# Kernel optimization log

Measured on AMD Instinct MI355X. Metric: run time of the kernel, lower is better.

The kernel has to match this reference:

```python
import jax, jax.numpy as jnp
import numpy as np

N = 50000   # nodes
E = 800000  # random edges (self-loops appended inside reference, as PyG GATConv does)
H = 4       # attention heads
LEAKY_SLOPE = 0.2
BN_EPS = 1e-5


def setup_inputs() -> dict:
    key = jax.random.key(0)
    ks = jax.random.split(key, 24)
    inp = {
        "x": jax.random.normal(ks[0], (N, 128), jnp.float32),
        "edge_index": jax.random.randint(ks[1], (2, E), 0, N, dtype=jnp.int64),
    }
    # layer dims: (in, out_per_head); concat -> out width = H*out
    dims = [(128, 64), (256, 64), (256, 32)]
    i = 2
    for l, (fin, c) in enumerate(dims, start=1):
        sc = 1.0 / np.sqrt(fin)
        inp[f"W{l}"] = jax.random.normal(ks[i], (fin, H * c), jnp.float32) * sc; i += 1
        inp[f"a_src{l}"] = jax.random.normal(ks[i], (H, c), jnp.float32) * 0.1; i += 1
        inp[f"a_dst{l}"] = jax.random.normal(ks[i], (H, c), jnp.float32) * 0.1; i += 1
        inp[f"b{l}"] = jnp.zeros((H * c,), jnp.float32)
    # batch norm params for the two non-final layers (width = 64*4 = 256)
    for l in (1, 2):
        inp[f"gamma{l}"] = jnp.ones((256,), jnp.float32)
        inp[f"beta{l}"] = jnp.zeros((256,), jnp.float32)
    return inp


def _gat_layer(x, src, dst, W, a_src, a_dst, b, heads):
    n = x.shape[0]
    h = (x @ W).reshape(n, heads, -1)                      # [N,H,C]
    al_s = jnp.sum(h * a_src, axis=-1)                     # [N,H]
    al_d = jnp.sum(h * a_dst, axis=-1)                     # [N,H]
    e = jax.nn.leaky_relu(al_s[src] + al_d[dst], LEAKY_SLOPE)  # [Etot,H]
    # numerically-stable edge softmax over incoming edges per destination
    m = jax.ops.segment_max(e, dst, num_segments=n)
    e = jnp.exp(e - m[dst])
    s = jax.ops.segment_sum(e, dst, num_segments=n)
    alpha = e / (s[dst] + 1e-16)                           # [Etot,H]
    msg = alpha[:, :, None] * h[src]                       # [Etot,H,C]
    out = jax.ops.segment_sum(msg, dst, num_segments=n)    # [N,H,C]
    out = out.reshape(n, -1) + b
    return jax.nn.relu(out)  # GAT_NET applies relu after conv


def _batch_norm(x, gamma, beta):
    mean = jnp.mean(x, axis=0)
    var = jnp.var(x, axis=0)  # biased, matches torch BN training normalization
    return (x - mean) * jax.lax.rsqrt(var + BN_EPS) * gamma + beta


def reference(x, edge_index, W1, a_src1, a_dst1, b1, gamma1, beta1,
              W2, a_src2, a_dst2, b2, gamma2, beta2,
              W3, a_src3, a_dst3, b3):
    n = x.shape[0]
    loop = jnp.arange(n, dtype=edge_index.dtype)
    src = jnp.concatenate([edge_index[0], loop])  # add self-loops (PyG default)
    dst = jnp.concatenate([edge_index[1], loop])

    h = _gat_layer(x, src, dst, W1, a_src1, a_dst1, b1, H)
    # outer F.relu is a no-op after GAT_NET's internal relu, kept implicitly
    h = _batch_norm(h, gamma1, beta1)

    h = _gat_layer(h, src, dst, W2, a_src2, a_dst2, b2, H)
    h = _batch_norm(h, gamma2, beta2)

    return _gat_layer(h, src, dst, W3, a_src3, a_dst3, b3, H)
```

## Files before the change

kernel.cpp:

```cpp
#include <hip/hip_runtime.h>
#include <hip/hip_bf16.h>

constexpr int NN   = 50000;
constexpr int EE   = 800000;
constexpr int ETOT = EE + NN;
constexpr int NP   = 50048;
constexpr int NBLK = (NN + 255) / 256;
constexpr float SLOPE  = 0.2f;
constexpr float EPS_BN = 1e-5f;

typedef __attribute__((ext_vector_type(8))) short bf16x8;
typedef __attribute__((ext_vector_type(4))) float f32x4;

__device__ inline float bf2f(unsigned short u) {
    union { unsigned int i; float f; } c; c.i = ((unsigned int)u) << 16; return c.f;
}

__device__ inline void gload16(const __hip_bfloat16* g, __hip_bfloat16* l) {
    __builtin_amdgcn_global_load_lds(
        (const __attribute__((address_space(1))) unsigned int*)g,
        (__attribute__((address_space(3))) unsigned int*)l, 16, 0, 0);
}


__global__ __launch_bounds__(256) void count_kernel(const int* __restrict__ ei,
                                                    int* __restrict__ cnt) {
    int j = blockIdx.x * 256 + threadIdx.x;
    if (j >= ETOT) return;
    int dst = (j < EE) ? ei[EE + j] : (j - EE);
    atomicAdd(&cnt[dst], 1);
}

__global__ __launch_bounds__(256) void scanA_kernel(const int* __restrict__ cnt,
                                                    int* __restrict__ off,
                                                    int* __restrict__ bsum) {
    int b = blockIdx.x, t = threadIdx.x;
    int i = b * 256 + t;
    int v = (i < NN) ? cnt[i] : 0;
    int lane = t & 63, w = t >> 6;
    int x = v;
    #pragma unroll
    for (int o = 1; o < 64; o <<= 1) { int y = __shfl_up(x, o); if (lane >= o) x += y; }
    __shared__ int ws[4];
    if (lane == 63) ws[w] = x;
    __syncthreads();
    int wo = 0;
    for (int k = 0; k < w; ++k) wo += ws[k];
    int incl = x + wo;
    if (i < NN) off[i] = incl - v;
    if (t == 255) bsum[b] = incl;
}

__global__ __launch_bounds__(256) void scanB_kernel(const int* __restrict__ bsum,
                                                    int* __restrict__ bexc,
                                                    int* __restrict__ off) {
    int t = threadIdx.x;
    int v = (t < NBLK) ? bsum[t] : 0;
    int lane = t & 63, w = t >> 6;
    int x = v;
    #pragma unroll
    for (int o = 1; o < 64; o <<= 1) { int y = __shfl_up(x, o); if (lane >= o) x += y; }
    __shared__ int ws[4];
    if (lane == 63) ws[w] = x;
    __syncthreads();
    int wo = 0;
    for (int k = 0; k < w; ++k) wo += ws[k];
    int incl = x + wo;
    if (t < NBLK) bexc[t] = incl - v;
    if (t == 255) off[NN] = incl;
}

__global__ __launch_bounds__(256) void scanC_kernel(const int* __restrict__ bexc,
                                                    int* __restrict__ off,
                                                    int* __restrict__ cur) {
    int i = blockIdx.x * 256 + threadIdx.x;
    if (i >= NN) return;
    int v = off[i] + bexc[blockIdx.x];
    off[i] = v;
    cur[i] = v;
}

__global__ __launch_bounds__(256) void fill_kernel(const int* __restrict__ ei,
                                                   int* __restrict__ cursor,
                                                   int* __restrict__ ssrc) {
    int j = blockIdx.x * 256 + threadIdx.x;
    if (j >= ETOT) return;
    int src, dst;
    if (j < EE) { src = ei[j]; dst = ei[EE + j]; }
    else        { src = dst = j - EE; }
    int pos = atomicAdd(&cursor[dst], 1);
    ssrc[pos] = src;
}

__global__ __launch_bounds__(256) void castx_kernel(const float* __restrict__ X,
                                                    __hip_bfloat16* __restrict__ Xbf) {
    long e0 = ((long)blockIdx.x * 256 + threadIdx.x) * 8;
    if (e0 >= (long)NP * 128) return;
    int row = (int)(e0 / 128);
    __hip_bfloat16 o[8];
    if (row < NN) {
        float4 v0 = *reinterpret_cast<const float4*>(X + e0);
        float4 v1 = *reinterpret_cast<const float4*>(X + e0 + 4);
        o[0] = __float2bfloat16(v0.x); o[1] = __float2bfloat16(v0.y);
        o[2] = __float2bfloat16(v0.z); o[3] = __float2bfloat16(v0.w);
        o[4] = __float2bfloat16(v1.x); o[5] = __float2bfloat16(v1.y);
        o[6] = __float2bfloat16(v1.z); o[7] = __float2bfloat16(v1.w);
    } else {
        for (int j = 0; j < 8; ++j) o[j] = __float2bfloat16(0.f);
    }
    *reinterpret_cast<bf16x8*>(Xbf + e0) = *reinterpret_cast<bf16x8*>(o);
}

__global__ __launch_bounds__(256) void castw1_kernel(const float* __restrict__ W,
                                                     __hip_bfloat16* __restrict__ WT) {
    int i = blockIdx.x * 256 + threadIdx.x;
    if (i >= 32768) return;
    int c = i / 128, k = i % 128;
    WT[i] = __float2bfloat16(W[(size_t)k * 256 + c]);
}

template <int FIN, int WOUT>
__global__ __launch_bounds__(FIN) void foldw_kernel(const float* __restrict__ W,
                                                    const float* __restrict__ scale,
                                                    const float* __restrict__ shift,
                                                    __hip_bfloat16* __restrict__ WTp,
                                                    float* __restrict__ bb) {
    int c = blockIdx.x, k = threadIdx.x;
    float w = W[(size_t)k * WOUT + c];
    WTp[(size_t)c * FIN + k] = __float2bfloat16(scale[k] * w);
    float p = shift[k] * w;
    #pragma unroll
    for (int o = 1; o < 64; o <<= 1) p += __shfl_xor(p, o);
    __shared__ float ps[FIN / 64];
    if ((k & 63) == 0) ps[k >> 6] = p;
    __syncthreads();
    if (k == 0) {
        float s = 0.f;
        #pragma unroll
        for (int q = 0; q < FIN / 64; ++q) s += ps[q];
        bb[c] = s;
    }
}

template <int FIN, int WOUT, bool FOLD>
__global__ __launch_bounds__(256) void mgemm_kernel(const __hip_bfloat16* __restrict__ A,
                                                    const __hip_bfloat16* __restrict__ BT,
                                                    const float* __restrict__ bb,
                                                    __hip_bfloat16* __restrict__ Hbf) {
    __shared__ __hip_bfloat16 As[128 * 32];
    __shared__ __hip_bfloat16 Bs[128 * 32];
    int t = threadIdx.x;
    int lane = t & 63, w = t >> 6;
    int row0 = blockIdx.x * 128;
    int col0 = blockIdx.y * 128;
    int wr = w >> 1, wc = w & 1;

    f32x4 acc[4][4];
    #pragma unroll
    for (int m = 0; m < 4; ++m)
        #pragma unroll
        for (int n = 0; n < 4; ++n) acc[m][n] = (f32x4){0.f, 0.f, 0.f, 0.f};

    int srow = w * 32 + (lane >> 2);
    int sbc  = (lane & 3) * 8;
    const __hip_bfloat16* gA0 = A  + (size_t)(row0 + srow)      * FIN + sbc;
    const __hip_bfloat16* gA1 = A  + (size_t)(row0 + srow + 16) * FIN + sbc;
    const __hip_bfloat16* gB0 = BT + (size_t)(col0 + srow)      * FIN + sbc;
    const __hip_bfloat16* gB1 = BT + (size_t)(col0 + srow + 16) * FIN + sbc;
    __hip_bfloat16* lA0 = As + w * 1024;
    __hip_bfloat16* lA1 = As + w * 1024 + 512;
    __hip_bfloat16* lB0 = Bs + w * 1024;
    __hip_bfloat16* lB1 = Bs + w * 1024 + 512;

    int rA = (wr * 64 + (lane & 15)) * 32 + (lane >> 4) * 8;
    int rB = (wc * 64 + (lane & 15)) * 32 + (lane >> 4) * 8;

    for (int k0 = 0; k0 < FIN; k0 += 32) {
        gload16(gA0 + k0, lA0);
        gload16(gA1 + k0, lA1);
        gload16(gB0 + k0, lB0);
        gload16(gB1 + k0, lB1);
        __syncthreads();
        bf16x8 af[4], bfr[4];
        #pragma unroll
        for (int m = 0; m < 4; ++m) af[m]  = *reinterpret_cast<const bf16x8*>(As + rA + m * 16 * 32);
        #pragma unroll
        for (int n = 0; n < 4; ++n) bfr[n] = *reinterpret_cast<const bf16x8*>(Bs + rB + n * 16 * 32);
        #pragma unroll
        for (int m = 0; m < 4; ++m)
            #pragma unroll
            for (int n = 0; n < 4; ++n)
                acc[m][n] = __builtin_amdgcn_mfma_f32_16x16x32_bf16(af[m], bfr[n], acc[m][n], 0, 0, 0);
        __syncthreads();
    }

    #pragma unroll
    for (int n = 0; n < 4; ++n) {
        int c = col0 + wc * 64 + n * 16 + (lane & 15);
        float badd = FOLD ? bb[c] : 0.f;
        #pragma unroll
        for (int m = 0; m < 4; ++m) {
            int r = row0 + wr * 64 + m * 16 + (lane >> 4) * 4;
            #pragma unroll
            for (int j = 0; j < 4; ++j)
                Hbf[(size_t)(r + j) * WOUT + c] = __float2bfloat16(acc[m][n][j] + badd);
        }
    }
}

template <int HC>
__global__ __launch_bounds__(256) void alsd_kernel(const __hip_bfloat16* __restrict__ Hm,
                                                   const float* __restrict__ a_src,
                                                   const float* __restrict__ a_dst,
                                                   float* __restrict__ als,
                                                   float* __restrict__ ald) {
    constexpr int VW = HC / 64;
    int wid  = threadIdx.x >> 6;
    int lane = threadIdx.x & 63;
    int node = blockIdx.x * 4 + wid;

    float ssum = 0.f, dsum = 0.f;
    if constexpr (VW == 4) {
        ushort4 h4 = *reinterpret_cast<const ushort4*>(Hm + (size_t)node * HC + lane * 4);
        float4 as = *reinterpret_cast<const float4*>(a_src + lane * 4);
        float4 ad = *reinterpret_cast<const float4*>(a_dst + lane * 4);
        float hx = bf2f(h4.x), hy = bf2f(h4.y), hz = bf2f(h4.z), hw = bf2f(h4.w);
        ssum = hx*as.x + hy*as.y + hz*as.z + hw*as.w;
        dsum = hx*ad.x + hy*ad.y + hz*ad.z + hw*ad.w;
    } else {
        ushort2 h2 = *reinterpret_cast<const ushort2*>(Hm + (size_t)node * HC + lane * 2);
        float2 as = *reinterpret_cast<const float2*>(a_src + lane * 2);
        float2 ad = *reinterpret_cast<const float2*>(a_dst + lane * 2);
        float hx = bf2f(h2.x), hy = bf2f(h2.y);
        ssum = hx*as.x + hy*as.y;
        dsum = hx*ad.x + hy*ad.y;
    }
    #pragma unroll
    for (int o = 1; o < 16; o <<= 1) {
        ssum += __shfl_xor(ssum, o);
        dsum += __shfl_xor(dsum, o);
    }
    if ((lane & 15) == 0) {
        int hd = lane >> 4;
        als[node * 4 + hd] = ssum;
        ald[node * 4 + hd] = dsum;
    }
}

template <int HC, bool OUTBF>
__global__ __launch_bounds__(256) void attn_kernel(const __hip_bfloat16* __restrict__ Hm,
                                                   const int* __restrict__ off,
                                                   const int* __restrict__ ssrc,
                                                   const float* __restrict__ als,
                                                   const float* __restrict__ ald,
                                                   const float* __restrict__ bias,
                                                   void* __restrict__ Outv) {
    constexpr int CPL = HC / 16;
    int wid  = threadIdx.x >> 6;
    int lane = threadIdx.x & 63;
    int d    = blockIdx.x * 4 + wid;
    int g    = lane >> 4;
    int q    = lane & 15;
    int head = q >> 2;

    int e0 = off[d], e1 = off[d + 1];
    float aldh = ald[(size_t)d * 4 + head];

    float acc0[CPL], acc1[CPL];
    #pragma unroll
    for (int c = 0; c < CPL; ++c) { acc0[c] = 0.f; acc1[c] = 0.f; }
    float den0 = 0.f, den1 = 0.f;

    int j = e0 + g;
    for (; j + 4 < e1; j += 8) {
        int s0 = ssrc[j];
        int s1 = ssrc[j + 4];
        float ea = als[(size_t)s0 * 4 + head] + aldh;
        ea = (ea > 0.f) ? ea : SLOPE * ea;
        float eb = als[(size_t)s1 * 4 + head] + aldh;
        eb = (eb > 0.f) ? eb : SLOPE * eb;
        float w0 = __expf(ea), w1 = __expf(eb);
        den0 += w0; den1 += w1;
        const __hip_bfloat16* hp0 = Hm + (size_t)s0 * HC + q * CPL;
        const __hip_bfloat16* hp1 = Hm + (size_t)s1 * HC + q * CPL;
        if constexpr (CPL == 16) {
            bf16x8 a0 = *reinterpret_cast<const bf16x8*>(hp0);
            bf16x8 a1 = *reinterpret_cast<const bf16x8*>(hp0 + 8);
            bf16x8 b0 = *reinterpret_cast<const bf16x8*>(hp1);
            bf16x8 b1 = *reinterpret_cast<const bf16x8*>(hp1 + 8);
            #pragma unroll
            for (int c = 0; c < 8; ++c) {
                acc0[c]     += w0 * bf2f((unsigned short)a0[c]);
                acc0[8 + c] += w0 * bf2f((unsigned short)a1[c]);
                acc1[c]     += w1 * bf2f((unsigned short)b0[c]);
                acc1[8 + c] += w1 * bf2f((unsigned short)b1[c]);
            }
        } else {
            bf16x8 a0 = *reinterpret_cast<const bf16x8*>(hp0);
            bf16x8 b0 = *reinterpret_cast<const bf16x8*>(hp1);
            #pragma unroll
            for (int c = 0; c < 8; ++c) {
                acc0[c] += w0 * bf2f((unsigned short)a0[c]);
                acc1[c] += w1 * bf2f((unsigned short)b0[c]);
            }
        }
    }
    if (j < e1) {
        int s0 = ssrc[j];
        float ea = als[(size_t)s0 * 4 + head] + aldh;
        ea = (ea > 0.f) ? ea : SLOPE * ea;
        float w0 = __expf(ea);
        den0 += w0;
        const __hip_bfloat16* hp0 = Hm + (size_t)s0 * HC + q * CPL;
        if constexpr (CPL == 16) {
            bf16x8 a0 = *reinterpret_cast<const bf16x8*>(hp0);
            bf16x8 a1 = *reinterpret_cast<const bf16x8*>(hp0 + 8);
            #pragma unroll
            for (int c = 0; c < 8; ++c) {
                acc0[c]     += w0 * bf2f((unsigned short)a0[c]);
                acc0[8 + c] += w0 * bf2f((unsigned short)a1[c]);
            }
        } else {
            bf16x8 a0 = *reinterpret_cast<const bf16x8*>(hp0);
            #pragma unroll
            for (int c = 0; c < 8; ++c) acc0[c] += w0 * bf2f((unsigned short)a0[c]);
        }
    }

    float den = den0 + den1;
    float acc[CPL];
    #pragma unroll
    for (int c = 0; c < CPL; ++c) acc[c] = acc0[c] + acc1[c];

    #pragma unroll
    for (int c = 0; c < CPL; ++c) {
        acc[c] += __shfl_xor(acc[c], 16);
        acc[c] += __shfl_xor(acc[c], 32);
    }
    den += __shfl_xor(den, 16);
    den += __shfl_xor(den, 32);
    float inv = 1.f / (den + 1e-16f);

    if (g == 0) {
        float o[CPL];
        #pragma unroll
        for (int c4 = 0; c4 < CPL / 4; ++c4) {
            float4 b4 = *reinterpret_cast<const float4*>(bias + q * CPL + c4 * 4);
            o[c4 * 4 + 0] = fmaxf(acc[c4 * 4 + 0] * inv + b4.x, 0.f);
            o[c4 * 4 + 1] = fmaxf(acc[c4 * 4 + 1] * inv + b4.y, 0.f);
            o[c4 * 4 + 2] = fmaxf(acc[c4 * 4 + 2] * inv + b4.z, 0.f);
            o[c4 * 4 + 3] = fmaxf(acc[c4 * 4 + 3] * inv + b4.w, 0.f);
        }
        if constexpr (OUTBF) {
            __hip_bfloat16 ob[CPL];
            #pragma unroll
            for (int c = 0; c < CPL; ++c) ob[c] = __float2bfloat16(o[c]);
            __hip_bfloat16* op = (__hip_bfloat16*)Outv + (size_t)d * HC + q * CPL;
            #pragma unroll
            for (int c8 = 0; c8 < CPL / 8; ++c8)
                *reinterpret_cast<bf16x8*>(op + c8 * 8) = *reinterpret_cast<bf16x8*>(ob + c8 * 8);
        } else {
            float* op = (float*)Outv + (size_t)d * HC + q * CPL;
            #pragma unroll
            for (int c4 = 0; c4 < CPL / 4; ++c4)
                *reinterpret_cast<float4*>(op + c4 * 4) =
                    make_float4(o[c4*4+0], o[c4*4+1], o[c4*4+2], o[c4*4+3]);
        }
    }
}

__global__ __launch_bounds__(256) void bnstats_kernel(const __hip_bfloat16* __restrict__ X,
                                                      float* __restrict__ sums) {
    int c  = threadIdx.x;
    int r0 = blockIdx.x * 200;
    float s = 0.f, q = 0.f;
    for (int r = r0; r < r0 + 200; ++r) {
        float v = bf2f(*(const unsigned short*)(X + (size_t)r * 256 + c));
        s += v; q += v * v;
    }
    atomicAdd(&sums[c], s);
    atomicAdd(&sums[256 + c], q);
}

__global__ __launch_bounds__(256) void bnfinal_kernel(const float* __restrict__ sums,
                                                      const float* __restrict__ gamma,
                                                      const float* __restrict__ beta,
                                                      float* __restrict__ scale,
                                                      float* __restrict__ shift) {
    int c = threadIdx.x;
    float mean = sums[c] / (float)NN;
    float var  = sums[256 + c] / (float)NN - mean * mean;
    float inv  = rsqrtf(var + EPS_BN);
    float sc   = gamma[c] * inv;
    scale[c] = sc;
    shift[c] = beta[c] - mean * sc;
}


extern "C" void kernel_launch(void* const* d_in, const int* in_sizes, int n_in,
                              void* d_out, int out_size, void* d_ws, size_t ws_size,
                              hipStream_t stream) {
    const float* x      = (const float*)d_in[0];
    const int*   ei     = (const int*)d_in[1];
    const float* W1     = (const float*)d_in[2];
    const float* a_s1   = (const float*)d_in[3];
    const float* a_d1   = (const float*)d_in[4];
    const float* b1     = (const float*)d_in[5];
    const float* W2     = (const float*)d_in[6];
    const float* a_s2   = (const float*)d_in[7];
    const float* a_d2   = (const float*)d_in[8];
    const float* b2     = (const float*)d_in[9];
    const float* W3     = (const float*)d_in[10];
    const float* a_s3   = (const float*)d_in[11];
    const float* a_d3   = (const float*)d_in[12];
    const float* b3     = (const float*)d_in[13];
    const float* gamma1 = (const float*)d_in[14];
    const float* beta1  = (const float*)d_in[15];
    const float* gamma2 = (const float*)d_in[16];
    const float* beta2  = (const float*)d_in[17];

    char* ws = (char*)d_ws;
    size_t o = 0;
    auto alloc = [&](size_t bytes) -> void* {
        void* p = ws + o;
        o = (o + bytes + 255) & ~size_t(255);
        return p;
    };
    __hip_bfloat16*  Abf  = (__hip_bfloat16*)alloc((size_t)NP * 256 * 2);
    __hip_bfloat16*  Hbf  = (__hip_bfloat16*)alloc((size_t)NP * 256 * 2);
    __hip_bfloat16*  Xbf  = (__hip_bfloat16*)alloc((size_t)NP * 128 * 2);
    __hip_bfloat16*  WT1  = (__hip_bfloat16*)alloc((size_t)256 * 128 * 2);
    __hip_bfloat16*  WT2  = (__hip_bfloat16*)alloc((size_t)256 * 256 * 2);
    __hip_bfloat16*  WT3  = (__hip_bfloat16*)alloc((size_t)128 * 256 * 2);
    float* bb2   = (float*)alloc(256 * 4);
    float* bb3   = (float*)alloc(128 * 4);
    float* als   = (float*)alloc((size_t)NN * 4 * 4);
    float* ald   = (float*)alloc((size_t)NN * 4 * 4);
    float* sums  = (float*)alloc(512 * 4);
    float* scale = (float*)alloc(256 * 4);
    float* shift = (float*)alloc(256 * 4);
    int*   off   = (int*)alloc((size_t)(NN + 1) * 4);
    int*   cur   = (int*)alloc((size_t)NN * 4);
    int*   cnt   = (int*)alloc((size_t)NN * 4);
    int*   bsum  = (int*)alloc((size_t)NBLK * 4);
    int*   bexc  = (int*)alloc((size_t)NBLK * 4);
    int*   ssrc  = (int*)alloc((size_t)ETOT * 4);
    (void)ws_size; (void)in_sizes; (void)n_in; (void)out_size;

    const int EB = (ETOT + 255) / 256;

    hipMemsetAsync(cnt, 0, (size_t)NN * 4, stream);
    count_kernel<<<EB, 256, 0, stream>>>(ei, cnt);
    scanA_kernel<<<NBLK, 256, 0, stream>>>(cnt, off, bsum);
    scanB_kernel<<<1, 256, 0, stream>>>(bsum, bexc, off);
    scanC_kernel<<<NBLK, 256, 0, stream>>>(bexc, off, cur);
    fill_kernel<<<EB, 256, 0, stream>>>(ei, cur, ssrc);

    castw1_kernel<<<128, 256, 0, stream>>>(W1, WT1);
    castx_kernel<<<(int)(((long)NP * 128 / 8 + 255) / 256), 256, 0, stream>>>(x, Xbf);
    mgemm_kernel<128, 256, false><<<dim3(NP / 128, 2), 256, 0, stream>>>(Xbf, WT1, nullptr, Hbf);
    alsd_kernel<256><<<NN / 4, 256, 0, stream>>>(Hbf, a_s1, a_d1, als, ald);
    attn_kernel<256, true><<<NN / 4, 256, 0, stream>>>(Hbf, off, ssrc, als, ald, b1, Abf);

    hipMemsetAsync(sums, 0, 512 * 4, stream);
    bnstats_kernel<<<250, 256, 0, stream>>>(Abf, sums);
    bnfinal_kernel<<<1, 256, 0, stream>>>(sums, gamma1, beta1, scale, shift);
    foldw_kernel<256, 256><<<256, 256, 0, stream>>>(W2, scale, shift, WT2, bb2);

    mgemm_kernel<256, 256, true><<<dim3(NP / 128, 2), 256, 0, stream>>>(Abf, WT2, bb2, Hbf);
    alsd_kernel<256><<<NN / 4, 256, 0, stream>>>(Hbf, a_s2, a_d2, als, ald);
    attn_kernel<256, true><<<NN / 4, 256, 0, stream>>>(Hbf, off, ssrc, als, ald, b2, Abf);

    hipMemsetAsync(sums, 0, 512 * 4, stream);
    bnstats_kernel<<<250, 256, 0, stream>>>(Abf, sums);
    bnfinal_kernel<<<1, 256, 0, stream>>>(sums, gamma2, beta2, scale, shift);
    foldw_kernel<256, 128><<<128, 256, 0, stream>>>(W3, scale, shift, WT3, bb3);

    mgemm_kernel<256, 128, true><<<dim3(NP / 128, 1), 256, 0, stream>>>(Abf, WT3, bb3, Hbf);
    alsd_kernel<128><<<NN / 4, 256, 0, stream>>>(Hbf, a_s3, a_d3, als, ald);
    attn_kernel<128, false><<<NN / 4, 256, 0, stream>>>(Hbf, off, ssrc, als, ald, b3, d_out);
}
```

Baseline: 402.5 us.

## Fuse attention-logit dot products into GEMM epilogue; one node per 16-lane group

Result: faster. 385.0 us (-4.3%).

```diff
diff --git a/kernel.cpp b/kernel.cpp
--- a/kernel.cpp
+++ b/kernel.cpp
@@ -146,7 +146,11 @@
 __global__ __launch_bounds__(256) void mgemm_kernel(const __hip_bfloat16* __restrict__ A,
                                                     const __hip_bfloat16* __restrict__ BT,
                                                     const float* __restrict__ bb,
-                                                    __hip_bfloat16* __restrict__ Hbf) {
+                                                    const float* __restrict__ a_src,
+                                                    const float* __restrict__ a_dst,
+                                                    __hip_bfloat16* __restrict__ Hbf,
+                                                    float* __restrict__ als,
+                                                    float* __restrict__ ald) {
     __shared__ __hip_bfloat16 As[128 * 32];
     __shared__ __hip_bfloat16 Bs[128 * 32];
     int t = threadIdx.x;
@@ -194,56 +198,86 @@
         __syncthreads();
     }
 
+    int cih = lane & 15;
+
+    if constexpr (FOLD) {
+        #pragma unroll
+        for (int n = 0; n < 4; ++n) {
+            float badd = bb[col0 + wc * 64 + n * 16 + cih];
+            #pragma unroll
+            for (int m = 0; m < 4; ++m)
+                #pragma unroll
+                for (int j = 0; j < 4; ++j) acc[m][n][j] += badd;
+        }
+    }
+
+    float asv[4], adv[4];
+    int headw = 0;
+    if constexpr (WOUT == 256) {
+        headw = (col0 >> 6) + wc;
+        #pragma unroll
+        for (int n = 0; n < 4; ++n) {
+            asv[n] = a_src[headw * 64 + n * 16 + cih];
+            adv[n] = a_dst[headw * 64 + n * 16 + cih];
+        }
+    } else {
+        #pragma unroll
+        for (int n = 0; n < 4; ++n) {
+            int hh = wc * 2 + (n >> 1);
+            asv[n] = a_src[hh * 32 + (n & 1) * 16 + cih];
+            adv[n] = a_dst[hh * 32 + (n & 1) * 16 + cih];
+        }
+    }
+
+    #pragma unroll
+    for (int m = 0; m < 4; ++m) {
+        #pragma unroll
+        for (int j = 0; j < 4; ++j) {
+            int r = row0 + wr * 64 + m * 16 + (lane >> 4) * 4 + j;
+            if constexpr (WOUT == 256) {
+                float vs = acc[m][0][j] * asv[0] + acc[m][1][j] * asv[1]
+                         + acc[m][2][j] * asv[2] + acc[m][3][j] * asv[3];
+                float vd = acc[m][0][j] * adv[0] + acc[m][1][j] * adv[1]
+                         + acc[m][2][j] * adv[2] + acc[m][3][j] * adv[3];
+                #pragma unroll
+                for (int o = 1; o < 16; o <<= 1) {
+                    vs += __shfl_xor(vs, o);
+                    vd += __shfl_xor(vd, o);
+                }
+                if (cih == 0) {
+                    als[(size_t)r * 4 + headw] = vs;
+                    ald[(size_t)r * 4 + headw] = vd;
+                }
+            } else {
+                float vs0 = acc[m][0][j] * asv[0] + acc[m][1][j] * asv[1];
+                float vs1 = acc[m][2][j] * asv[2] + acc[m][3][j] * asv[3];
+                float vd0 = acc[m][0][j] * adv[0] + acc[m][1][j] * adv[1];
+                float vd1 = acc[m][2][j] * adv[2] + acc[m][3][j] * adv[3];
+                #pragma unroll
+                for (int o = 1; o < 16; o <<= 1) {
+                    vs0 += __shfl_xor(vs0, o); vs1 += __shfl_xor(vs1, o);
+                    vd0 += __shfl_xor(vd0, o); vd1 += __shfl_xor(vd1, o);
+                }
+                if (cih == 0) {
+                    als[(size_t)r * 4 + wc * 2]     = vs0;
+                    als[(size_t)r * 4 + wc * 2 + 1] = vs1;
+                    ald[(size_t)r * 4 + wc * 2]     = vd0;
+                    ald[(size_t)r * 4 + wc * 2 + 1] = vd1;
+                }
+            }
+        }
+    }
+
     #pragma unroll
     for (int n = 0; n < 4; ++n) {
-        int c = col0 + wc * 64 + n * 16 + (lane & 15);
-        float badd = FOLD ? bb[c] : 0.f;
+        int c = col0 + wc * 64 + n * 16 + cih;
         #pragma unroll
         for (int m = 0; m < 4; ++m) {
             int r = row0 + wr * 64 + m * 16 + (lane >> 4) * 4;
             #pragma unroll
             for (int j = 0; j < 4; ++j)
-                Hbf[(size_t)(r + j) * WOUT + c] = __float2bfloat16(acc[m][n][j] + badd);
-        }
-    }
-}
-
-template <int HC>
-__global__ __launch_bounds__(256) void alsd_kernel(const __hip_bfloat16* __restrict__ Hm,
-                                                   const float* __restrict__ a_src,
-                                                   const float* __restrict__ a_dst,
-                                                   float* __restrict__ als,
-                                                   float* __restrict__ ald) {
-    constexpr int VW = HC / 64;
-    int wid  = threadIdx.x >> 6;
-    int lane = threadIdx.x & 63;
-    int node = blockIdx.x * 4 + wid;
-
-    float ssum = 0.f, dsum = 0.f;
-    if constexpr (VW == 4) {
-        ushort4 h4 = *reinterpret_cast<const ushort4*>(Hm + (size_t)node * HC + lane * 4);
-        float4 as = *reinterpret_cast<const float4*>(a_src + lane * 4);
-        float4 ad = *reinterpret_cast<const float4*>(a_dst + lane * 4);
-        float hx = bf2f(h4.x), hy = bf2f(h4.y), hz = bf2f(h4.z), hw = bf2f(h4.w);
-        ssum = hx*as.x + hy*as.y + hz*as.z + hw*as.w;
-        dsum = hx*ad.x + hy*ad.y + hz*ad.z + hw*ad.w;
-    } else {
-        ushort2 h2 = *reinterpret_cast<const ushort2*>(Hm + (size_t)node * HC + lane * 2);
-        float2 as = *reinterpret_cast<const float2*>(a_src + lane * 2);
-        float2 ad = *reinterpret_cast<const float2*>(a_dst + lane * 2);
-        float hx = bf2f(h2.x), hy = bf2f(h2.y);
-        ssum = hx*as.x + hy*as.y;
-        dsum = hx*ad.x + hy*ad.y;
-    }
-    #pragma unroll
-    for (int o = 1; o < 16; o <<= 1) {
-        ssum += __shfl_xor(ssum, o);
-        dsum += __shfl_xor(dsum, o);
-    }
-    if ((lane & 15) == 0) {
-        int hd = lane >> 4;
-        als[node * 4 + hd] = ssum;
-        ald[node * 4 + hd] = dsum;
+                Hbf[(size_t)(r + j) * WOUT + c] = __float2bfloat16(acc[m][n][j]);
+        }
     }
 }
 
@@ -258,114 +292,110 @@
     constexpr int CPL = HC / 16;
     int wid  = threadIdx.x >> 6;
     int lane = threadIdx.x & 63;
-    int d    = blockIdx.x * 4 + wid;
     int g    = lane >> 4;
     int q    = lane & 15;
+    int d    = blockIdx.x * 16 + wid * 4 + g;
     int head = q >> 2;
 
     int e0 = off[d], e1 = off[d + 1];
     float aldh = ald[(size_t)d * 4 + head];
 
-    float acc0[CPL], acc1[CPL];
-    #pragma unroll
-    for (int c = 0; c < CPL; ++c) { acc0[c] = 0.f; acc1[c] = 0.f; }
-    float den0 = 0.f, den1 = 0.f;
-
-    int j = e0 + g;
-    for (; j + 4 < e1; j += 8) {
-        int s0 = ssrc[j];
-        int s1 = ssrc[j + 4];
-        float ea = als[(size_t)s0 * 4 + head] + aldh;
-        ea = (ea > 0.f) ? ea : SLOPE * ea;
-        float eb = als[(size_t)s1 * 4 + head] + aldh;
-        eb = (eb > 0.f) ? eb : SLOPE * eb;
-        float w0 = __expf(ea), w1 = __expf(eb);
-        den0 += w0; den1 += w1;
-        const __hip_bfloat16* hp0 = Hm + (size_t)s0 * HC + q * CPL;
-        const __hip_bfloat16* hp1 = Hm + (size_t)s1 * HC + q * CPL;
+    float acc[CPL];
+    #pragma unroll
+    for (int c = 0; c < CPL; ++c) acc[c] = 0.f;
+    float den = 0.f;
+
+    int j = e0;
+    for (; j + 3 < e1; j += 4) {
+        int s0 = ssrc[j], s1 = ssrc[j + 1], s2 = ssrc[j + 2], s3 = ssrc[j + 3];
+        float x0 = als[(size_t)s0 * 4 + head] + aldh;
+        float x1 = als[(size_t)s1 * 4 + head] + aldh;
+        float x2 = als[(size_t)s2 * 4 + head] + aldh;
+        float x3 = als[(size_t)s3 * 4 + head] + aldh;
+        x0 = (x0 > 0.f) ? x0 : SLOPE * x0;
+        x1 = (x1 > 0.f) ? x1 : SLOPE * x1;
+        x2 = (x2 > 0.f) ? x2 : SLOPE * x2;
+        x3 = (x3 > 0.f) ? x3 : SLOPE * x3;
+        float w0 = __expf(x0), w1 = __expf(x1), w2 = __expf(x2), w3 = __expf(x3);
+        den += (w0 + w1) + (w2 + w3);
+        const __hip_bfloat16* p0 = Hm + (size_t)s0 * HC + q * CPL;
+        const __hip_bfloat16* p1 = Hm + (size_t)s1 * HC + q * CPL;
+        const __hip_bfloat16* p2 = Hm + (size_t)s2 * HC + q * CPL;
+        const __hip_bfloat16* p3 = Hm + (size_t)s3 * HC + q * CPL;
         if constexpr (CPL == 16) {
-            bf16x8 a0 = *reinterpret_cast<const bf16x8*>(hp0);
-            bf16x8 a1 = *reinterpret_cast<const bf16x8*>(hp0 + 8);
-            bf16x8 b0 = *reinterpret_cast<const bf16x8*>(hp1);
-            bf16x8 b1 = *reinterpret_cast<const bf16x8*>(hp1 + 8);
+            bf16x8 a0 = *reinterpret_cast<const bf16x8*>(p0);
+            bf16x8 a1 = *reinterpret_cast<const bf16x8*>(p0 + 8);
+            bf16x8 b0 = *reinterpret_cast<const bf16x8*>(p1);
+            bf16x8 b1 = *reinterpret_cast<const bf16x8*>(p1 + 8);
+            bf16x8 c0 = *reinterpret_cast<const bf16x8*>(p2);
+            bf16x8 c1 = *reinterpret_cast<const bf16x8*>(p2 + 8);
+            bf16x8 d0 = *reinterpret_cast<const bf16x8*>(p3);
+            bf16x8 d1 = *reinterpret_cast<const bf16x8*>(p3 + 8);
             #pragma unroll
             for (int c = 0; c < 8; ++c) {
-                acc0[c]     += w0 * bf2f((unsigned short)a0[c]);
-                acc0[8 + c] += w0 * bf2f((unsigned short)a1[c]);
-                acc1[c]     += w1 * bf2f((unsigned short)b0[c]);
-                acc1[8 + c] += w1 * bf2f((unsigned short)b1[c]);
+                acc[c]     += w0 * bf2f((unsigned short)a0[c]) + w1 * bf2f((unsigned short)b0[c])
+                            + w2 * bf2f((unsigned short)c0[c]) + w3 * bf2f((unsigned short)d0[c]);
+                acc[8 + c] += w0 * bf2f((unsigned short)a1[c]) + w1 * bf2f((unsigned short)b1[c])
+                            + w2 * bf2f((unsigned short)c1[c]) + w3 * bf2f((unsigned short)d1[c]);
             }
         } else {
-            bf16x8 a0 = *reinterpret_cast<const bf16x8*>(hp0);
-            bf16x8 b0 = *reinterpret_cast<const bf16x8*>(hp1);
+            bf16x8 a0 = *reinterpret_cast<const bf16x8*>(p0);
+            bf16x8 b0 = *reinterpret_cast<const bf16x8*>(p1);
+            bf16x8 c0 = *reinterpret_cast<const bf16x8*>(p2);
+            bf16x8 d0 = *reinterpret_cast<const bf16x8*>(p3);
+            #pragma unroll
+            for (int c = 0; c < 8; ++c)
+                acc[c] += w0 * bf2f((unsigned short)a0[c]) + w1 * bf2f((unsigned short)b0[c])
+                        + w2 * bf2f((unsigned short)c0[c]) + w3 * bf2f((unsigned short)d0[c]);
+        }
+    }
+    for (; j < e1; ++j) {
+        int s0 = ssrc[j];
+        float x0 = als[(size_t)s0 * 4 + head] + aldh;
+        x0 = (x0 > 0.f) ? x0 : SLOPE * x0;
+        float w0 = __expf(x0);
+        den += w0;
+        const __hip_bfloat16* p0 = Hm + (size_t)s0 * HC + q * CPL;
+        if constexpr (CPL == 16) {
+            bf16x8 a0 = *reinterpret_cast<const bf16x8*>(p0);
+            bf16x8 a1 = *reinterpret_cast<const bf16x8*>(p0 + 8);
             #pragma unroll
             for (int c = 0; c < 8; ++c) {
-                acc0[c] += w0 * bf2f((unsigned short)a0[c]);
-                acc1[c] += w1 * bf2f((unsigned short)b0[c]);
-            }
-        }
-    }
-    if (j < e1) {
-        int s0 = ssrc[j];
-        float ea = als[(size_t)s0 * 4 + head] + aldh;
-        ea = (ea > 0.f) ? ea : SLOPE * ea;
-        float w0 = __expf(ea);
-        den0 += w0;
-        const __hip_bfloat16* hp0 = Hm + (size_t)s0 * HC + q * CPL;
-        if constexpr (CPL == 16) {
-            bf16x8 a0 = *reinterpret_cast<const bf16x8*>(hp0);
-            bf16x8 a1 = *reinterpret_cast<const bf16x8*>(hp0 + 8);
-            #pragma unroll
-            for (int c = 0; c < 8; ++c) {
-                acc0[c]     += w0 * bf2f((unsigned short)a0[c]);
-                acc0[8 + c] += w0 * bf2f((unsigned short)a1[c]);
+                acc[c]     += w0 * bf2f((unsigned short)a0[c]);
+                acc[8 + c] += w0 * bf2f((unsigned short)a1[c]);
             }
         } else {
-            bf16x8 a0 = *reinterpret_cast<const bf16x8*>(hp0);
-            #pragma unroll
-            for (int c = 0; c < 8; ++c) acc0[c] += w0 * bf2f((unsigned short)a0[c]);
-        }
-    }
-
-    float den = den0 + den1;
-    float acc[CPL];
-    #pragma unroll
-    for (int c = 0; c < CPL; ++c) acc[c] = acc0[c] + acc1[c];
-
-    #pragma unroll
-    for (int c = 0; c < CPL; ++c) {
-        acc[c] += __shfl_xor(acc[c], 16);
-        acc[c] += __shfl_xor(acc[c], 32);
-    }
-    den += __shfl_xor(den, 16);
-    den += __shfl_xor(den, 32);
+            bf16x8 a0 = *reinterpret_cast<const bf16x8*>(p0);
+            #pragma unroll
+            for (int c = 0; c < 8; ++c) acc[c] += w0 * bf2f((unsigned short)a0[c]);
+        }
+    }
+
     float inv = 1.f / (den + 1e-16f);
 
-    if (g == 0) {
-        float o[CPL];
-        #pragma unroll
-        for (int c4 = 0; c4 < CPL / 4; ++c4) {
-            float4 b4 = *reinterpret_cast<const float4*>(bias + q * CPL + c4 * 4);
-            o[c4 * 4 + 0] = fmaxf(acc[c4 * 4 + 0] * inv + b4.x, 0.f);
-            o[c4 * 4 + 1] = fmaxf(acc[c4 * 4 + 1] * inv + b4.y, 0.f);
-            o[c4 * 4 + 2] = fmaxf(acc[c4 * 4 + 2] * inv + b4.z, 0.f);
-            o[c4 * 4 + 3] = fmaxf(acc[c4 * 4 + 3] * inv + b4.w, 0.f);
-        }
-        if constexpr (OUTBF) {
-            __hip_bfloat16 ob[CPL];
-            #pragma unroll
-            for (int c = 0; c < CPL; ++c) ob[c] = __float2bfloat16(o[c]);
-            __hip_bfloat16* op = (__hip_bfloat16*)Outv + (size_t)d * HC + q * CPL;
-            #pragma unroll
-            for (int c8 = 0; c8 < CPL / 8; ++c8)
-                *reinterpret_cast<bf16x8*>(op + c8 * 8) = *reinterpret_cast<bf16x8*>(ob + c8 * 8);
-        } else {
-            float* op = (float*)Outv + (size_t)d * HC + q * CPL;
-            #pragma unroll
-            for (int c4 = 0; c4 < CPL / 4; ++c4)
-                *reinterpret_cast<float4*>(op + c4 * 4) =
-                    make_float4(o[c4*4+0], o[c4*4+1], o[c4*4+2], o[c4*4+3]);
-        }
+    float o[CPL];
+    #pragma unroll
+    for (int c4 = 0; c4 < CPL / 4; ++c4) {
+        float4 b4 = *reinterpret_cast<const float4*>(bias + q * CPL + c4 * 4);
+        o[c4 * 4 + 0] = fmaxf(acc[c4 * 4 + 0] * inv + b4.x, 0.f);
+        o[c4 * 4 + 1] = fmaxf(acc[c4 * 4 + 1] * inv + b4.y, 0.f);
+        o[c4 * 4 + 2] = fmaxf(acc[c4 * 4 + 2] * inv + b4.z, 0.f);
+        o[c4 * 4 + 3] = fmaxf(acc[c4 * 4 + 3] * inv + b4.w, 0.f);
+    }
+    if constexpr (OUTBF) {
+        __hip_bfloat16 ob[CPL];
+        #pragma unroll
+        for (int c = 0; c < CPL; ++c) ob[c] = __float2bfloat16(o[c]);
+        __hip_bfloat16* op = (__hip_bfloat16*)Outv + (size_t)d * HC + q * CPL;
+        #pragma unroll
+        for (int c8 = 0; c8 < CPL / 8; ++c8)
+            *reinterpret_cast<bf16x8*>(op + c8 * 8) = *reinterpret_cast<bf16x8*>(ob + c8 * 8);
+    } else {
+        float* op = (float*)Outv + (size_t)d * HC + q * CPL;
+        #pragma unroll
+        for (int c4 = 0; c4 < CPL / 4; ++c4)
+            *reinterpret_cast<float4*>(op + c4 * 4) =
+                make_float4(o[c4*4+0], o[c4*4+1], o[c4*4+2], o[c4*4+3]);
     }
 }
 
@@ -434,8 +464,8 @@
     __hip_bfloat16*  WT3  = (__hip_bfloat16*)alloc((size_t)128 * 256 * 2);
     float* bb2   = (float*)alloc(256 * 4);
     float* bb3   = (float*)alloc(128 * 4);
-    float* als   = (float*)alloc((size_t)NN * 4 * 4);
-    float* ald   = (float*)alloc((size_t)NN * 4 * 4);
+    float* als   = (float*)alloc((size_t)NP * 4 * 4);
+    float* ald   = (float*)alloc((size_t)NP * 4 * 4);
     float* sums  = (float*)alloc(512 * 4);
     float* scale = (float*)alloc(256 * 4);
     float* shift = (float*)alloc(256 * 4);
@@ -458,25 +488,25 @@
 
     castw1_kernel<<<128, 256, 0, stream>>>(W1, WT1);
     castx_kernel<<<(int)(((long)NP * 128 / 8 + 255) / 256), 256, 0, stream>>>(x, Xbf);
-    mgemm_kernel<128, 256, false><<<dim3(NP / 128, 2), 256, 0, stream>>>(Xbf, WT1, nullptr, Hbf);
-    alsd_kernel<256><<<NN / 4, 256, 0, stream>>>(Hbf, a_s1, a_d1, als, ald);
-    attn_kernel<256, true><<<NN / 4, 256, 0, stream>>>(Hbf, off, ssrc, als, ald, b1, Abf);
+    mgemm_kernel<128, 256, false><<<dim3(NP / 128, 2), 256, 0, stream>>>(
+        Xbf, WT1, nullptr, a_s1, a_d1, Hbf, als, ald);
+    attn_kernel<256, true><<<NN / 16, 256, 0, stream>>>(Hbf, off, ssrc, als, ald, b1, Abf);
 
     hipMemsetAsync(sums, 0, 512 * 4, stream);
     bnstats_kernel<<<250, 256, 0, stream>>>(Abf, sums);
     bnfinal_kernel<<<1, 256, 0, stream>>>(sums, gamma1, beta1, scale, shift);
     foldw_kernel<256, 256><<<256, 256, 0, stream>>>(W2, scale, shift, WT2, bb2);
 
-    mgemm_kernel<256, 256, true><<<dim3(NP / 128, 2), 256, 0, stream>>>(Abf, WT2, bb2, Hbf);
-    alsd_kernel<256><<<NN / 4, 256, 0, stream>>>(Hbf, a_s2, a_d2, als, ald);
-    attn_kernel<256, true><<<NN / 4, 256, 0, stream>>>(Hbf, off, ssrc, als, ald, b2, Abf);
+    mgemm_kernel<256, 256, true><<<dim3(NP / 128, 2), 256, 0, stream>>>(
+        Abf, WT2, bb2, a_s2, a_d2, Hbf, als, ald);
+    attn_kernel<256, true><<<NN / 16, 256, 0, stream>>>(Hbf, off, ssrc, als, ald, b2, Abf);
 
     hipMemsetAsync(sums, 0, 512 * 4, stream);
     bnstats_kernel<<<250, 256, 0, stream>>>(Abf, sums);
     bnfinal_kernel<<<1, 256, 0, stream>>>(sums, gamma2, beta2, scale, shift);
     foldw_kernel<256, 128><<<128, 256, 0, stream>>>(W3, scale, shift, WT3, bb3);
 
-    mgemm_kernel<256, 128, true><<<dim3(NP / 128, 1), 256, 0, stream>>>(Abf, WT3, bb3, Hbf);
-    alsd_kernel<128><<<NN / 4, 256, 0, stream>>>(Hbf, a_s3, a_d3, als, ald);
-    attn_kernel<128, false><<<NN / 4, 256, 0, stream>>>(Hbf, off, ssrc, als, ald, b3, d_out);
-}
+    mgemm_kernel<256, 128, true><<<dim3(NP / 128, 1), 256, 0, stream>>>(
+        Abf, WT3, bb3, a_s3, a_d3, Hbf, als, ald);
+    attn_kernel<128, false><<<NN / 16, 256, 0, stream>>>(Hbf, off, ssrc, als, ald, b3, d_out);
+}
```
